# Performance work log

Measured on AMD Instinct MI355X. Metric: run time of the kernel, lower is better.

The kernel has to match this reference:

```python
import jax, jax.numpy as jnp
import numpy as np

B, L, D, H = 8, 1024, 768, 12
UNITS, NHEADS, HDIM = 768, 12, 64
R = 0.5  # ours_force_reduction_ratio
NEG = jnp.finfo(jnp.float32).min


def setup_inputs() -> dict:
    key = jax.random.key(0)
    ks = jax.random.split(key, 12)
    hidden_states = jax.random.normal(ks[0], (B, L, D), jnp.float32)
    # HF-style extended attention mask [B,1,1,L]: 0 for valid, big negative for padding
    lengths = jax.random.randint(ks[1], (B,), L // 2, L + 1)
    pos = jnp.arange(L)
    attention_mask = jnp.where(pos[None, :] < lengths[:, None], 0.0, -1e9).astype(jnp.float32).reshape(B, 1, 1, L)
    self_attention_scores = jax.random.uniform(ks[2], (B, H, L, L), dtype=jnp.float32)
    key_layer = jax.random.normal(ks[3], (B, H, L, HDIM), jnp.float32)  # unused by forward
    tome_size = jnp.ones((B, L, 1), jnp.float32)  # unused by forward (recomputed)
    s = 0.02
    Wq = jax.random.normal(ks[4], (D, UNITS), jnp.float32) * s
    Wk = jax.random.normal(ks[5], (D, UNITS), jnp.float32) * s
    Wv = jax.random.normal(ks[6], (D, UNITS), jnp.float32) * s
    Wo = jax.random.normal(ks[7], (UNITS, D), jnp.float32) * s
    bq = jnp.zeros((UNITS,), jnp.float32)
    bk = jnp.zeros((UNITS,), jnp.float32)
    bv = jnp.zeros((UNITS,), jnp.float32)
    bo = jnp.zeros((D,), jnp.float32)
    return dict(hidden_states=hidden_states, attention_mask=attention_mask,
                self_attention_scores=self_attention_scores, key_layer=key_layer,
                tome_size=tome_size, Wq=Wq, bq=bq, Wk=Wk, bk=bk, Wv=Wv, bv=bv, Wo=Wo, bo=bo)


def _mha(q, kv, key_padding_mask, Wq, bq, Wk, bk, Wv, bv, Wo, bo):
    # standard multi-head cross attention; q: [B,Lq,D], kv: [B,L,D]
    Bq, Lq, _ = q.shape
    Q = (q @ Wq + bq).reshape(Bq, Lq, NHEADS, HDIM)
    Kp = (kv @ Wk + bk).reshape(Bq, -1, NHEADS, HDIM)
    Vp = (kv @ Wv + bv).reshape(Bq, -1, NHEADS, HDIM)
    scores = jnp.einsum('bqhd,bkhd->bhqk', Q, Kp) / jnp.sqrt(jnp.float32(HDIM))
    if key_padding_mask is not None:
        scores = jnp.where(key_padding_mask[:, None, None, :], NEG, scores)
    att = jax.nn.softmax(scores, axis=-1)
    out = jnp.einsum('bhqk,bkhd->bqhd', att, Vp).reshape(Bq, Lq, UNITS)
    return out @ Wo + bo


def reference(hidden_states, attention_mask, self_attention_scores, key_layer, tome_size,
              Wq, bq, Wk, bk, Wv, bv, Wo, bo):
    # per-sample variable K = floor(valid_len * R) - num_new_token, clamped to >= 1
    valid = (attention_mask > -10.0).astype(hidden_states.dtype)  # [B,1,1,L]
    K_list = (valid.reshape(B, L).sum(-1) * R).astype(jnp.int32)
    K_list = jnp.maximum(K_list - 1, 1)  # num_new_token == 1
    # masked_attention_scores: outer product of the 0/1 mask applied per head
    m = valid.reshape(B, L)
    scores = self_attention_scores * (m[:, :, None] * m[:, None, :])[:, None, :, :]
    imp = scores.mean(axis=1).mean(axis=1)  # mean over heads then queries -> [B,L]
    imp = imp.at[:, 0].set(jnp.inf)  # always preserve CLS
    # rank of each token in descending importance (double argsort)
    order = jnp.argsort(-imp, axis=-1)
    rank = jnp.argsort(order, axis=-1)
    keep = rank < K_list[:, None]  # [B,L]; topk_attention_mask == ~keep
    preserved_attention_mask = jnp.where(keep[:, None, None, :], attention_mask, NEG)
    # sentence pooling via softmax over the extended mask
    att = jax.nn.softmax(attention_mask, axis=-1).reshape(B, 1, L)
    sentences = jnp.einsum('bql,bld->bqd', att, hidden_states)  # [B,1,D]
    key_padding_mask = attention_mask.reshape(B, L) < -10.0
    new_token = _mha(sentences, hidden_states, key_padding_mask, Wq, bq, Wk, bk, Wv, bv, Wo, bo)
    final_token = jnp.concatenate([hidden_states, new_token], axis=1)  # [B,L+1,D]
    new_attention_mask = jnp.zeros((B, 1, 1, 1), hidden_states.dtype)
    final_attention_mask = jnp.concatenate([preserved_attention_mask, new_attention_mask], axis=-1)
    tome = jnp.ones((B, L + 1, 1), hidden_states.dtype)
    return final_token, final_attention_mask, tome
```

## Files before the change

### kernel.cpp

```cpp
#include <hip/hip_runtime.h>
#include <math.h>

#define Bb 8
#define Ll 1024
#define Dd 768
#define Hh 12
#define ROWS7 32
#define QS 8
#define SS 8
#define WSC 16
#define DC 24

#define NIMP (Bb*Hh*QS)
#define NSENT (Bb*SS)
#define NCOPY4 (Bb*Ll*Dd/4)
#define NTOME4 (Bb*(Ll+1)/4)
#define NCPYBLK ((NCOPY4 + NTOME4 + 255)/256)
#define GRID_A (NIMP + NSENT + NCPYBLK + 1)

__device__ __constant__ float NEGF_ = -3.0e38f;

#define OFF_COUNTS   0
#define OFF_QPART    256
#define OFF_QV       (OFF_QPART + DC*Bb*Dd*4)
#define OFF_U        (OFF_QV + Bb*Dd*4)
#define OFF_SBUF     (OFF_U + Bb*Hh*Dd*4)
#define OFF_SENTP    (OFF_SBUF + (size_t)Bb*Hh*Ll*4)
#define OFF_PART     (OFF_SENTP + Bb*SS*Dd*8)
#define OFF_WPART    (OFF_PART + (size_t)Bb*Hh*QS*Ll*4)
#define OFF_OPART    (OFF_WPART + (size_t)Bb*WSC*Hh*Dd*4)
#define OFF_NPART    (OFF_OPART + DC*Bb*Dd*4)

__device__ __forceinline__ int block_count256(const float* __restrict__ amask_b, int t) {
    int c = 0;
    #pragma unroll
    for (int i = 0; i < 4; ++i)
        c += (amask_b[t + 256*i] > -10.0f) ? 1 : 0;
    #pragma unroll
    for (int off = 32; off; off >>= 1) c += __shfl_xor(c, off, 64);
    __shared__ int cred[4];
    if ((t & 63) == 0) cred[t >> 6] = c;
    __syncthreads();
    return cred[0] + cred[1] + cred[2] + cred[3];
}

__global__ void kA_mega(const float4* __restrict__ scores4, const float* __restrict__ amask,
                        const float4* __restrict__ hid4,
                        float4* __restrict__ part4, double* __restrict__ sentp,
                        int* __restrict__ counts, float4* __restrict__ out4) {
    int blk = blockIdx.x;
    int t = threadIdx.x;
    if (blk < NIMP) {
        int b = blk / (Hh*QS);
        int rem = blk % (Hh*QS);
        int h = rem / QS, c = rem % QS;
        int count = block_count256(amask + b*Ll, t);
        int rpc = (count + QS - 1) / QS;
        int q0 = c*rpc, q1 = min(q0 + rpc, count);
        const float4* base = scores4 + ((size_t)(b*Hh + h)*Ll)*(Ll/4) + t;
        float ax=0.f, ay=0.f, az=0.f, aw=0.f;
        float bx=0.f, by=0.f, bz=0.f, bw=0.f;
        int q = q0;
        #pragma unroll 4
        for (; q + 1 < q1; q += 2) {
            float4 v0 = base[(size_t)q*(Ll/4)];
            float4 v1 = base[(size_t)(q+1)*(Ll/4)];
            ax += v0.x; ay += v0.y; az += v0.z; aw += v0.w;
            bx += v1.x; by += v1.y; bz += v1.z; bw += v1.w;
        }
        if (q < q1) {
            float4 v = base[(size_t)q*(Ll/4)];
            ax += v.x; ay += v.y; az += v.z; aw += v.w;
        }
        float4 o; o.x = ax+bx; o.y = ay+by; o.z = az+bz; o.w = aw+bw;
        part4[(size_t)(b*(Hh*QS) + rem)*(Ll/4) + t] = o;
    } else if (blk < NIMP + NSENT) {
        int blk2 = blk - NIMP;
        int b = blk2 / SS, c = blk2 % SS;
        int count = block_count256(amask + b*Ll, t);
        int rpc = (count + SS - 1) / SS;
        int l0 = c*rpc, l1 = min(l0 + rpc, count);
        if (t < 192) {
            double a0=0, a1=0, a2=0, a3=0;
            const float4* base = hid4 + (size_t)b*Ll*(Dd/4) + t;
            #pragma unroll 4
            for (int l = l0; l < l1; ++l) {
                float4 v = base[(size_t)l*(Dd/4)];
                a0 += (double)v.x; a1 += (double)v.y; a2 += (double)v.z; a3 += (double)v.w;
            }
            double* o = sentp + (size_t)(b*SS + c)*Dd + 4*t;
            o[0]=a0; o[1]=a1; o[2]=a2; o[3]=a3;
        }
    } else if (blk < NIMP + NSENT + NCPYBLK) {
        int idx = (blk - NIMP - NSENT)*256 + t;
        if (idx < NCOPY4) {
            int b = idx / (Ll*Dd/4), r = idx % (Ll*Dd/4);
            out4[(size_t)b*((Ll+1)*Dd/4) + r] = hid4[idx];
        } else if (idx < NCOPY4 + NTOME4) {
            float4 one; one.x=one.y=one.z=one.w = 1.0f;
            out4[(size_t)(Bb*(Ll+1)*Dd + Bb*(Ll+1))/4 + (idx - NCOPY4)] = one;
        }
    } else {
        int w = t >> 6, lane = t & 63;
        for (int b = w; b < Bb; b += 4) {
            int c = 0;
            #pragma unroll
            for (int i = 0; i < 16; ++i)
                c += (amask[b*Ll + lane + 64*i] > -10.0f) ? 1 : 0;
            #pragma unroll
            for (int off = 32; off; off >>= 1) c += __shfl_xor(c, off, 64);
            if (lane == 0) counts[b] = c;
        }
    }
}

__global__ void kB_rank(const float* __restrict__ part, const int* __restrict__ counts,
                        const float* __restrict__ amask, float* __restrict__ out_mask) {
    __shared__ double simp[Ll];
    int blk = blockIdx.x;
    int b = blk >> 4, seg = blk & 15;
    int t = threadIdx.x;
    int count = counts[b];
    #pragma unroll
    for (int i = 0; i < 4; ++i) {
        int k = t + 256*i;
        double v;
        if (k == 0) v = 1.0e300;
        else if (k < count) {
            double s = 0.0;
            #pragma unroll 4
            for (int j = 0; j < Hh*QS; ++j)
                s += (double)part[(size_t)(b*(Hh*QS) + j)*Ll + k];
            v = s * (1.0/12288.0);
        } else v = 0.0;
        simp[k] = v;
    }
    __syncthreads();
    int K = max((count >> 1) - 1, 1);
    int ti = seg*64 + (t >> 2);
    int prt = t & 3;
    double mv = simp[ti];
    int cnt = 0;
    int l0 = prt*256;
    #pragma unroll 4
    for (int j = 0; j < 256; ++j) {
        int l = l0 + j;
        double v = simp[l];
        cnt += (v > mv || (v == mv && l < ti)) ? 1 : 0;
    }
    cnt += __shfl_xor(cnt, 1, 64);
    cnt += __shfl_xor(cnt, 2, 64);
    if (prt == 0)
        out_mask[b*(Ll+1) + ti] = (cnt < K) ? amask[b*Ll + ti] : NEGF_;
    if (seg == 0 && t == 0) out_mask[b*(Ll+1) + Ll] = 0.0f;
}

__global__ void kC_qpart(const double* __restrict__ sentp, const int* __restrict__ counts,
                         const float* __restrict__ Wq, float* __restrict__ qpart) {
    __shared__ float s_lds[Bb][32];
    int blk = blockIdx.x, t = threadIdx.x;
    int d0 = blk*32;
    {
        int b = t >> 5, dd = t & 31;
        double s = 0.0;
        #pragma unroll
        for (int c = 0; c < SS; ++c)
            s += sentp[(size_t)(b*SS + c)*Dd + d0 + dd];
        s_lds[b][dd] = (float)(s / (double)counts[b]);
    }
    __syncthreads();
    float acc[Bb][3];
    #pragma unroll
    for (int b = 0; b < Bb; ++b) { acc[b][0]=0.f; acc[b][1]=0.f; acc[b][2]=0.f; }
    #pragma unroll 4
    for (int dd = 0; dd < 32; ++dd) {
        const float* wr = Wq + (size_t)(d0 + dd)*Dd;
        float w0 = wr[t], w1 = wr[t+256], w2 = wr[t+512];
        #pragma unroll
        for (int b = 0; b < Bb; ++b) {
            float sv = s_lds[b][dd];
            acc[b][0] += sv*w0; acc[b][1] += sv*w1; acc[b][2] += sv*w2;
        }
    }
    #pragma unroll
    for (int b = 0; b < Bb; ++b) {
        float* o = qpart + (size_t)(blk*Bb + b)*Dd;
        o[t] = acc[b][0]; o[t+256] = acc[b][1]; o[t+512] = acc[b][2];
    }
}

__global__ void kD_u(const float* __restrict__ qpart, const float* __restrict__ bq,
                     const float* __restrict__ Wk,
                     float* __restrict__ Qv, float* __restrict__ u) {
    __shared__ float q_lds[64];
    int blk = blockIdx.x; int b = blk / Hh, h = blk % Hh;
    int t = threadIdx.x;
    if (t < 64) {
        int j = h*64 + t;
        float s = 0.f;
        #pragma unroll
        for (int c = 0; c < DC; ++c) s += qpart[(size_t)(c*Bb + b)*Dd + j];
        s += bq[j];
        q_lds[t] = s;
        Qv[b*Dd + j] = s;
    }
    __syncthreads();
    #pragma unroll
    for (int i = 0; i < 3; ++i) {
        int d = t + 256*i;
        const float* wr = Wk + (size_t)d*Dd + h*64;
        float acc = 0.f;
        #pragma unroll
        for (int j = 0; j < 64; ++j) acc += wr[j]*q_lds[j];
        u[(size_t)(b*Hh + h)*Dd + d] = acc;
    }
}

__global__ void kE_scores(const float4* __restrict__ hid4, const float4* __restrict__ u4,
                          const float* __restrict__ Qv, const float* __restrict__ bk,
                          const int* __restrict__ counts, float* __restrict__ sbuf) {
    __shared__ float4 u_lds[Hh*192];
    __shared__ float qbk[Hh];
    int blk = blockIdx.x;
    int b = blk / (Ll/ROWS7);
    int kc = blk % (Ll/ROWS7);
    int t = threadIdx.x;
    for (int i = t; i < Hh*192; i += 256) u_lds[i] = u4[(size_t)b*Hh*192 + i];
    if (t < Hh) {
        float a = 0.f;
        for (int j = 0; j < 64; ++j) a += Qv[b*Dd + t*64 + j] * bk[t*64 + j];
        qbk[t] = a;
    }
    __syncthreads();
    int count = counts[b];
    int wave = t >> 6, lane = t & 63;
    #pragma unroll
    for (int r = 0; r < ROWS7/4; ++r) {
        int k = kc*ROWS7 + wave + 4*r;
        const float4* hr4 = hid4 + (size_t)(b*Ll + k)*(Dd/4) + lane;
        float a[Hh];
        #pragma unroll
        for (int h = 0; h < Hh; ++h) a[h] = 0.f;
        #pragma unroll
        for (int i = 0; i < 3; ++i) {
            float4 v = hr4[i*64];
            #pragma unroll
            for (int h = 0; h < Hh; ++h) {
                float4 uv = u_lds[h*192 + i*64 + lane];
                a[h] += v.x*uv.x + v.y*uv.y + v.z*uv.z + v.w*uv.w;
            }
        }
        #pragma unroll
        for (int h = 0; h < Hh; ++h) {
            #pragma unroll
            for (int off = 32; off; off >>= 1) a[h] += __shfl_xor(a[h], off, 64);
        }
        #pragma unroll
        for (int h = 0; h < Hh; ++h) {
            if (lane == h) {
                sbuf[(size_t)(b*Hh + h)*Ll + k] =
                    (k < count) ? (a[h] + qbk[h]) * 0.125f : -1.0e30f;
            }
        }
    }
}

__global__ void kF_softmax(float* __restrict__ sbuf) {
    __shared__ float redmax[4];
    __shared__ float redsum[4];
    int blk = blockIdx.x, t = threadIdx.x;
    float* s = sbuf + (size_t)blk * Ll;
    int wave = t >> 6, lane = t & 63;
    float v0 = s[t], v1 = s[t+256], v2 = s[t+512], v3 = s[t+768];
    float mx = fmaxf(fmaxf(v0, v1), fmaxf(v2, v3));
    #pragma unroll
    for (int off = 32; off; off >>= 1) mx = fmaxf(mx, __shfl_xor(mx, off, 64));
    if (lane == 0) redmax[wave] = mx;
    __syncthreads();
    mx = fmaxf(fmaxf(redmax[0], redmax[1]), fmaxf(redmax[2], redmax[3]));
    float e0 = expf(v0-mx), e1 = expf(v1-mx), e2 = expf(v2-mx), e3 = expf(v3-mx);
    float sum = e0+e1+e2+e3;
    #pragma unroll
    for (int off = 32; off; off >>= 1) sum += __shfl_xor(sum, off, 64);
    if (lane == 0) redsum[wave] = sum;
    __syncthreads();
    sum = redsum[0]+redsum[1]+redsum[2]+redsum[3];
    s[t]     = e0/sum;
    s[t+256] = e1/sum;
    s[t+512] = e2/sum;
    s[t+768] = e3/sum;
}

__global__ void kG_wpart(const float4* __restrict__ hid4, const float* __restrict__ att,
                         const int* __restrict__ counts, float4* __restrict__ wpart4) {
    __shared__ float att_s[Hh][64];
    int blk = blockIdx.x;
    int b = blk / WSC, c = blk % WSC;
    int count = counts[b];
    int rpc = (count + WSC - 1) / WSC;
    int l0 = c*rpc, l1 = min(l0 + rpc, count);
    int nl = l1 - l0;
    int t = threadIdx.x;
    for (int idx = t; idx < Hh*64; idx += 192) {
        int h = idx >> 6, ll = idx & 63;
        att_s[h][ll] = (ll < nl) ? att[(size_t)(b*Hh + h)*Ll + l0 + ll] : 0.f;
    }
    __syncthreads();
    float4 acc[Hh];
    #pragma unroll
    for (int h = 0; h < Hh; ++h) { acc[h].x=0.f; acc[h].y=0.f; acc[h].z=0.f; acc[h].w=0.f; }
    const float4* base = hid4 + (size_t)b*Ll*(Dd/4) + t;
    #pragma unroll 2
    for (int l = 0; l < nl; ++l) {
        float4 v = base[(size_t)(l0 + l)*(Dd/4)];
        #pragma unroll
        for (int h = 0; h < Hh; ++h) {
            float ah = att_s[h][l];
            acc[h].x += ah*v.x; acc[h].y += ah*v.y; acc[h].z += ah*v.z; acc[h].w += ah*v.w;
        }
    }
    #pragma unroll
    for (int h = 0; h < Hh; ++h)
        wpart4[((size_t)(b*WSC + c)*Hh + h)*(Dd/4) + t] = acc[h];
}

__global__ void kH_opart(const float* __restrict__ wpart, const float* __restrict__ Wv,
                         float* __restrict__ opart) {
    __shared__ float w_lds[Bb][Hh][32];
    int blk = blockIdx.x, t = threadIdx.x;
    int d0 = blk*32;
    for (int idx = t; idx < Bb*Hh*32; idx += 256) {
        int b = idx / (Hh*32);
        int rem = idx % (Hh*32);
        int h = rem >> 5, dd = rem & 31;
        float s = 0.f;
        #pragma unroll
        for (int c = 0; c < WSC; ++c)
            s += wpart[((size_t)(b*WSC + c)*Hh + h)*Dd + d0 + dd];
        w_lds[b][h][dd] = s;
    }
    __syncthreads();
    int j0 = t, j1 = t+256, j2 = t+512;
    int h0 = j0 >> 6, h1 = j1 >> 6, h2 = j2 >> 6;
    float acc[Bb][3];
    #pragma unroll
    for (int b = 0; b < Bb; ++b) { acc[b][0]=0.f; acc[b][1]=0.f; acc[b][2]=0.f; }
    #pragma unroll 4
    for (int dd = 0; dd < 32; ++dd) {
        const float* wr = Wv + (size_t)(d0 + dd)*Dd;
        float w0 = wr[j0], w1 = wr[j1], w2 = wr[j2];
        #pragma unroll
        for (int b = 0; b < Bb; ++b) {
            acc[b][0] += w_lds[b][h0][dd]*w0;
            acc[b][1] += w_lds[b][h1][dd]*w1;
            acc[b][2] += w_lds[b][h2][dd]*w2;
        }
    }
    #pragma unroll
    for (int b = 0; b < Bb; ++b) {
        float* o = opart + (size_t)(blk*Bb + b)*Dd;
        o[j0] = acc[b][0]; o[j1] = acc[b][1]; o[j2] = acc[b][2];
    }
}

__global__ void kI_npart(const float* __restrict__ opart, const float* __restrict__ bv,
                         const float* __restrict__ Wo, float* __restrict__ npart) {
    __shared__ float o_lds[Bb][32];
    int blk = blockIdx.x, t = threadIdx.x;
    int jr0 = blk*32;
    {
        int b = t >> 5, jj = t & 31;
        int j = jr0 + jj;
        float s = 0.f;
        #pragma unroll
        for (int c = 0; c < DC; ++c) s += opart[(size_t)(c*Bb + b)*Dd + j];
        o_lds[b][jj] = s + bv[j];
    }
    __syncthreads();
    float acc[Bb][3];
    #pragma unroll
    for (int b = 0; b < Bb; ++b) { acc[b][0]=0.f; acc[b][1]=0.f; acc[b][2]=0.f; }
    #pragma unroll 4
    for (int jj = 0; jj < 32; ++jj) {
        const float* wr = Wo + (size_t)(jr0 + jj)*Dd;
        float w0 = wr[t], w1 = wr[t+256], w2 = wr[t+512];
        #pragma unroll
        for (int b = 0; b < Bb; ++b) {
            float ov = o_lds[b][jj];
            acc[b][0] += ov*w0; acc[b][1] += ov*w1; acc[b][2] += ov*w2;
        }
    }
    #pragma unroll
    for (int b = 0; b < Bb; ++b) {
        float* o = npart + (size_t)(blk*Bb + b)*Dd;
        o[t] = acc[b][0]; o[t+256] = acc[b][1]; o[t+512] = acc[b][2];
    }
}

__global__ void kJ_final(const float* __restrict__ npart, const float* __restrict__ bo,
                         float* __restrict__ out) {
    int b = blockIdx.x, t = threadIdx.x;
    size_t base = ((size_t)b*(Ll+1) + Ll)*Dd;
    #pragma unroll
    for (int i = 0; i < 3; ++i) {
        int d = t + 256*i;
        float s = 0.f;
        #pragma unroll
        for (int c = 0; c < DC; ++c) s += npart[(size_t)(c*Bb + b)*Dd + d];
        out[base + d] = s + bo[d];
    }
}

extern "C" void kernel_launch(void* const* d_in, const int* in_sizes, int n_in,
                              void* d_out, int out_size, void* d_ws, size_t ws_size,
                              hipStream_t stream) {
    const float* hidden = (const float*)d_in[0];
    const float* amask  = (const float*)d_in[1];
    const float* scores = (const float*)d_in[2];
    const float* Wq = (const float*)d_in[5];
    const float* bq = (const float*)d_in[6];
    const float* Wk = (const float*)d_in[7];
    const float* bk = (const float*)d_in[8];
    const float* Wv = (const float*)d_in[9];
    const float* bv = (const float*)d_in[10];
    const float* Wo = (const float*)d_in[11];
    const float* bo = (const float*)d_in[12];
    float* out = (float*)d_out;

    char* ws = (char*)d_ws;
    int*    counts = (int*)   (ws + OFF_COUNTS);
    float*  qpart  = (float*) (ws + OFF_QPART);
    float*  Qv     = (float*) (ws + OFF_QV);
    float*  u      = (float*) (ws + OFF_U);
    float*  sbuf   = (float*) (ws + OFF_SBUF);
    double* sentp  = (double*)(ws + OFF_SENTP);
    float*  part   = (float*) (ws + OFF_PART);
    float*  wpart  = (float*) (ws + OFF_WPART);
    float*  opart  = (float*) (ws + OFF_OPART);
    float*  npart  = (float*) (ws + OFF_NPART);

    float* out_mask = out + (size_t)Bb*(Ll+1)*Dd;

    kA_mega   <<<GRID_A, 256, 0, stream>>>((const float4*)scores, amask,
                                           (const float4*)hidden,
                                           (float4*)part, sentp, counts, (float4*)out);
    kB_rank   <<<Bb*16, 256, 0, stream>>>(part, counts, amask, out_mask);
    kC_qpart  <<<DC, 256, 0, stream>>>(sentp, counts, Wq, qpart);
    kD_u      <<<Bb*Hh, 256, 0, stream>>>(qpart, bq, Wk, Qv, u);
    kE_scores <<<Bb*(Ll/ROWS7), 256, 0, stream>>>((const float4*)hidden, (const float4*)u,
                                                  Qv, bk, counts, sbuf);
    kF_softmax<<<Bb*Hh, 256, 0, stream>>>(sbuf);
    kG_wpart  <<<Bb*WSC, 192, 0, stream>>>((const float4*)hidden, sbuf, counts,
                                           (float4*)wpart);
    kH_opart  <<<DC, 256, 0, stream>>>(wpart, Wv, opart);
    kI_npart  <<<DC, 256, 0, stream>>>(opart, bv, Wo, npart);
    kJ_final  <<<Bb, 256, 0, stream>>>(npart, bo, out);
}
```

Baseline: 209.6 us.

## Fuse small attention stages, fold softmax into wpart, skip padded score columns

```diff
diff --git a/kernel.cpp b/kernel.cpp
--- a/kernel.cpp
+++ b/kernel.cpp
@@ -21,15 +21,13 @@
 __device__ __constant__ float NEGF_ = -3.0e38f;
 
 #define OFF_COUNTS   0
-#define OFF_QPART    256
-#define OFF_QV       (OFF_QPART + DC*Bb*Dd*4)
-#define OFF_U        (OFF_QV + Bb*Dd*4)
-#define OFF_SBUF     (OFF_U + Bb*Hh*Dd*4)
-#define OFF_SENTP    (OFF_SBUF + (size_t)Bb*Hh*Ll*4)
-#define OFF_PART     (OFF_SENTP + Bb*SS*Dd*8)
-#define OFF_WPART    (OFF_PART + (size_t)Bb*Hh*QS*Ll*4)
-#define OFF_OPART    (OFF_WPART + (size_t)Bb*WSC*Hh*Dd*4)
-#define OFF_NPART    (OFF_OPART + DC*Bb*Dd*4)
+#define OFF_QBK      256
+#define OFF_OBUF     1024
+#define OFF_U        25600
+#define OFF_SENTP    320512
+#define OFF_SBUF     713728
+#define OFF_PART     1106944
+#define OFF_WPART    4252672
 
 __device__ __forceinline__ int block_count256(const float* __restrict__ amask_b, int t) {
     int c = 0;
@@ -57,6 +55,7 @@
         int count = block_count256(amask + b*Ll, t);
         int rpc = (count + QS - 1) / QS;
         int q0 = c*rpc, q1 = min(q0 + rpc, count);
+        if (4*t >= count) return;
         const float4* base = scores4 + ((size_t)(b*Hh + h)*Ll)*(Ll/4) + t;
         float ax=0.f, ay=0.f, az=0.f, aw=0.f;
         float bx=0.f, by=0.f, bz=0.f, bw=0.f;
@@ -114,123 +113,110 @@
     }
 }
 
-__global__ void kB_rank(const float* __restrict__ part, const int* __restrict__ counts,
-                        const float* __restrict__ amask, float* __restrict__ out_mask) {
+__global__ void kBCD(const float* __restrict__ part, const double* __restrict__ sentp,
+                     const int* __restrict__ counts, const float* __restrict__ amask,
+                     const float* __restrict__ Wq, const float* __restrict__ bq,
+                     const float* __restrict__ Wk, const float* __restrict__ bk,
+                     float* __restrict__ out_mask, float* __restrict__ u,
+                     float* __restrict__ qbk) {
     __shared__ double simp[Ll];
+    __shared__ float s_lds[Dd];
+    __shared__ float qpart_lds[4][64];
+    __shared__ float q_lds[64];
     int blk = blockIdx.x;
-    int b = blk >> 4, seg = blk & 15;
     int t = threadIdx.x;
-    int count = counts[b];
-    #pragma unroll
-    for (int i = 0; i < 4; ++i) {
-        int k = t + 256*i;
-        double v;
-        if (k == 0) v = 1.0e300;
-        else if (k < count) {
+    if (blk < 128) {
+        int b = blk >> 4, seg = blk & 15;
+        int count = counts[b];
+        #pragma unroll
+        for (int i = 0; i < 4; ++i) {
+            int k = t + 256*i;
+            double v;
+            if (k == 0) v = 1.0e300;
+            else if (k < count) {
+                double s = 0.0;
+                #pragma unroll 4
+                for (int j = 0; j < Hh*QS; ++j)
+                    s += (double)part[(size_t)(b*(Hh*QS) + j)*Ll + k];
+                v = s * (1.0/12288.0);
+            } else v = 0.0;
+            simp[k] = v;
+        }
+        __syncthreads();
+        int K = max((count >> 1) - 1, 1);
+        int ti = seg*64 + (t >> 2);
+        int prt = t & 3;
+        double mv = simp[ti];
+        int cnt = 0;
+        int l0 = prt*256;
+        #pragma unroll 4
+        for (int j = 0; j < 256; ++j) {
+            int l = l0 + j;
+            double v = simp[l];
+            cnt += (v > mv || (v == mv && l < ti)) ? 1 : 0;
+        }
+        cnt += __shfl_xor(cnt, 1, 64);
+        cnt += __shfl_xor(cnt, 2, 64);
+        if (prt == 0)
+            out_mask[b*(Ll+1) + ti] = (cnt < K) ? amask[b*Ll + ti] : NEGF_;
+        if (seg == 0 && t == 0) out_mask[b*(Ll+1) + Ll] = 0.0f;
+    } else {
+        int idx = blk - 128;
+        int b = idx / Hh, h = idx % Hh;
+        double cntd = (double)counts[b];
+        for (int i = t; i < Dd; i += 256) {
             double s = 0.0;
+            #pragma unroll
+            for (int c = 0; c < SS; ++c) s += sentp[(size_t)(b*SS + c)*Dd + i];
+            s_lds[i] = (float)(s / cntd);
+        }
+        __syncthreads();
+        {
+            int j = t & 63, g = t >> 6;
+            float acc = 0.f;
+            const float* wq = Wq + h*64 + j;
+            int d0 = g*192;
             #pragma unroll 4
-            for (int j = 0; j < Hh*QS; ++j)
-                s += (double)part[(size_t)(b*(Hh*QS) + j)*Ll + k];
-            v = s * (1.0/12288.0);
-        } else v = 0.0;
-        simp[k] = v;
-    }
-    __syncthreads();
-    int K = max((count >> 1) - 1, 1);
-    int ti = seg*64 + (t >> 2);
-    int prt = t & 3;
-    double mv = simp[ti];
-    int cnt = 0;
-    int l0 = prt*256;
-    #pragma unroll 4
-    for (int j = 0; j < 256; ++j) {
-        int l = l0 + j;
-        double v = simp[l];
-        cnt += (v > mv || (v == mv && l < ti)) ? 1 : 0;
-    }
-    cnt += __shfl_xor(cnt, 1, 64);
-    cnt += __shfl_xor(cnt, 2, 64);
-    if (prt == 0)
-        out_mask[b*(Ll+1) + ti] = (cnt < K) ? amask[b*Ll + ti] : NEGF_;
-    if (seg == 0 && t == 0) out_mask[b*(Ll+1) + Ll] = 0.0f;
-}
-
-__global__ void kC_qpart(const double* __restrict__ sentp, const int* __restrict__ counts,
-                         const float* __restrict__ Wq, float* __restrict__ qpart) {
-    __shared__ float s_lds[Bb][32];
-    int blk = blockIdx.x, t = threadIdx.x;
-    int d0 = blk*32;
-    {
-        int b = t >> 5, dd = t & 31;
-        double s = 0.0;
-        #pragma unroll
-        for (int c = 0; c < SS; ++c)
-            s += sentp[(size_t)(b*SS + c)*Dd + d0 + dd];
-        s_lds[b][dd] = (float)(s / (double)counts[b]);
-    }
-    __syncthreads();
-    float acc[Bb][3];
-    #pragma unroll
-    for (int b = 0; b < Bb; ++b) { acc[b][0]=0.f; acc[b][1]=0.f; acc[b][2]=0.f; }
-    #pragma unroll 4
-    for (int dd = 0; dd < 32; ++dd) {
-        const float* wr = Wq + (size_t)(d0 + dd)*Dd;
-        float w0 = wr[t], w1 = wr[t+256], w2 = wr[t+512];
-        #pragma unroll
-        for (int b = 0; b < Bb; ++b) {
-            float sv = s_lds[b][dd];
-            acc[b][0] += sv*w0; acc[b][1] += sv*w1; acc[b][2] += sv*w2;
-        }
-    }
-    #pragma unroll
-    for (int b = 0; b < Bb; ++b) {
-        float* o = qpart + (size_t)(blk*Bb + b)*Dd;
-        o[t] = acc[b][0]; o[t+256] = acc[b][1]; o[t+512] = acc[b][2];
-    }
-}
-
-__global__ void kD_u(const float* __restrict__ qpart, const float* __restrict__ bq,
-                     const float* __restrict__ Wk,
-                     float* __restrict__ Qv, float* __restrict__ u) {
-    __shared__ float q_lds[64];
-    int blk = blockIdx.x; int b = blk / Hh, h = blk % Hh;
-    int t = threadIdx.x;
-    if (t < 64) {
-        int j = h*64 + t;
-        float s = 0.f;
-        #pragma unroll
-        for (int c = 0; c < DC; ++c) s += qpart[(size_t)(c*Bb + b)*Dd + j];
-        s += bq[j];
-        q_lds[t] = s;
-        Qv[b*Dd + j] = s;
-    }
-    __syncthreads();
-    #pragma unroll
-    for (int i = 0; i < 3; ++i) {
-        int d = t + 256*i;
-        const float* wr = Wk + (size_t)d*Dd + h*64;
-        float acc = 0.f;
-        #pragma unroll
-        for (int j = 0; j < 64; ++j) acc += wr[j]*q_lds[j];
-        u[(size_t)(b*Hh + h)*Dd + d] = acc;
+            for (int d = d0; d < d0 + 192; ++d)
+                acc += s_lds[d] * wq[(size_t)d*Dd];
+            qpart_lds[g][j] = acc;
+        }
+        __syncthreads();
+        if (t < 64) {
+            float q = qpart_lds[0][t] + qpart_lds[1][t] + qpart_lds[2][t]
+                    + qpart_lds[3][t] + bq[h*64 + t];
+            q_lds[t] = q;
+        }
+        __syncthreads();
+        if (t == 0) {
+            float a = 0.f;
+            #pragma unroll
+            for (int jj = 0; jj < 64; ++jj) a += q_lds[jj]*bk[h*64 + jj];
+            qbk[b*Hh + h] = a;
+        }
+        #pragma unroll
+        for (int i = 0; i < 3; ++i) {
+            int d = t + 256*i;
+            const float* wr = Wk + (size_t)d*Dd + h*64;
+            float acc = 0.f;
+            #pragma unroll
+            for (int jj = 0; jj < 64; ++jj) acc += wr[jj]*q_lds[jj];
+            u[(size_t)(b*Hh + h)*Dd + d] = acc;
+        }
     }
 }
 
 __global__ void kE_scores(const float4* __restrict__ hid4, const float4* __restrict__ u4,
-                          const float* __restrict__ Qv, const float* __restrict__ bk,
-                          const int* __restrict__ counts, float* __restrict__ sbuf) {
+                          const float* __restrict__ qbk, const int* __restrict__ counts,
+                          float* __restrict__ sbuf) {
     __shared__ float4 u_lds[Hh*192];
-    __shared__ float qbk[Hh];
+    __shared__ float qbk_lds[Hh];
     int blk = blockIdx.x;
     int b = blk / (Ll/ROWS7);
     int kc = blk % (Ll/ROWS7);
     int t = threadIdx.x;
     for (int i = t; i < Hh*192; i += 256) u_lds[i] = u4[(size_t)b*Hh*192 + i];
-    if (t < Hh) {
-        float a = 0.f;
-        for (int j = 0; j < 64; ++j) a += Qv[b*Dd + t*64 + j] * bk[t*64 + j];
-        qbk[t] = a;
-    }
+    if (t < Hh) qbk_lds[t] = qbk[b*Hh + t];
     __syncthreads();
     int count = counts[b];
     int wave = t >> 6, lane = t & 63;
@@ -259,51 +245,46 @@
         for (int h = 0; h < Hh; ++h) {
             if (lane == h) {
                 sbuf[(size_t)(b*Hh + h)*Ll + k] =
-                    (k < count) ? (a[h] + qbk[h]) * 0.125f : -1.0e30f;
+                    (k < count) ? (a[h] + qbk_lds[h]) * 0.125f : -1.0e30f;
             }
         }
     }
 }
 
-__global__ void kF_softmax(float* __restrict__ sbuf) {
-    __shared__ float redmax[4];
-    __shared__ float redsum[4];
-    int blk = blockIdx.x, t = threadIdx.x;
-    float* s = sbuf + (size_t)blk * Ll;
-    int wave = t >> 6, lane = t & 63;
-    float v0 = s[t], v1 = s[t+256], v2 = s[t+512], v3 = s[t+768];
-    float mx = fmaxf(fmaxf(v0, v1), fmaxf(v2, v3));
-    #pragma unroll
-    for (int off = 32; off; off >>= 1) mx = fmaxf(mx, __shfl_xor(mx, off, 64));
-    if (lane == 0) redmax[wave] = mx;
-    __syncthreads();
-    mx = fmaxf(fmaxf(redmax[0], redmax[1]), fmaxf(redmax[2], redmax[3]));
-    float e0 = expf(v0-mx), e1 = expf(v1-mx), e2 = expf(v2-mx), e3 = expf(v3-mx);
-    float sum = e0+e1+e2+e3;
-    #pragma unroll
-    for (int off = 32; off; off >>= 1) sum += __shfl_xor(sum, off, 64);
-    if (lane == 0) redsum[wave] = sum;
-    __syncthreads();
-    sum = redsum[0]+redsum[1]+redsum[2]+redsum[3];
-    s[t]     = e0/sum;
-    s[t+256] = e1/sum;
-    s[t+512] = e2/sum;
-    s[t+768] = e3/sum;
-}
-
-__global__ void kG_wpart(const float4* __restrict__ hid4, const float* __restrict__ att,
-                         const int* __restrict__ counts, float4* __restrict__ wpart4) {
+__global__ void kGp_wpart(const float4* __restrict__ hid4, const float* __restrict__ sbuf,
+                          const int* __restrict__ counts, float4* __restrict__ wpart4) {
+    __shared__ float m_s[Hh], is_s[Hh];
     __shared__ float att_s[Hh][64];
     int blk = blockIdx.x;
     int b = blk / WSC, c = blk % WSC;
+    int t = threadIdx.x;
+    int wave = t >> 6, lane = t & 63;
+    #pragma unroll
+    for (int i = 0; i < 4; ++i) {
+        int h = wave*4 + i;
+        const float* s = sbuf + (size_t)(b*Hh + h)*Ll;
+        float vals[16];
+        float mx = -INFINITY;
+        #pragma unroll
+        for (int q = 0; q < 16; ++q) { vals[q] = s[lane + 64*q]; mx = fmaxf(mx, vals[q]); }
+        #pragma unroll
+        for (int off = 32; off; off >>= 1) mx = fmaxf(mx, __shfl_xor(mx, off, 64));
+        float sum = 0.f;
+        #pragma unroll
+        for (int q = 0; q < 16; ++q) sum += expf(vals[q] - mx);
+        #pragma unroll
+        for (int off = 32; off; off >>= 1) sum += __shfl_xor(sum, off, 64);
+        if (lane == 0) { m_s[h] = mx; is_s[h] = 1.f/sum; }
+    }
+    __syncthreads();
     int count = counts[b];
     int rpc = (count + WSC - 1) / WSC;
     int l0 = c*rpc, l1 = min(l0 + rpc, count);
     int nl = l1 - l0;
-    int t = threadIdx.x;
     for (int idx = t; idx < Hh*64; idx += 192) {
         int h = idx >> 6, ll = idx & 63;
-        att_s[h][ll] = (ll < nl) ? att[(size_t)(b*Hh + h)*Ll + l0 + ll] : 0.f;
+        att_s[h][ll] = (ll < nl)
+            ? expf(sbuf[(size_t)(b*Hh + h)*Ll + l0 + ll] - m_s[h]) * is_s[h] : 0.f;
     }
     __syncthreads();
     float4 acc[Hh];
@@ -324,91 +305,66 @@
         wpart4[((size_t)(b*WSC + c)*Hh + h)*(Dd/4) + t] = acc[h];
 }
 
-__global__ void kH_opart(const float* __restrict__ wpart, const float* __restrict__ Wv,
-                         float* __restrict__ opart) {
-    __shared__ float w_lds[Bb][Hh][32];
+__global__ void kHp_out(const float* __restrict__ wpart, const float* __restrict__ Wv,
+                        const float* __restrict__ bv, float* __restrict__ obuf) {
+    __shared__ float w_lds[Bb][Dd];
+    __shared__ float red[8][32][Bb];
+    int blk = blockIdx.x, t = threadIdx.x;
+    int h = blk >> 1, j0 = blk*32;
+    for (int idx = t; idx < Bb*Dd; idx += 256) {
+        int b = idx / Dd, d = idx % Dd;
+        float s = 0.f;
+        #pragma unroll
+        for (int c = 0; c < WSC; ++c)
+            s += wpart[((size_t)(b*WSC + c)*Hh + h)*Dd + d];
+        w_lds[b][d] = s;
+    }
+    __syncthreads();
+    int jj = t & 31, g = t >> 5;
+    float acc[Bb];
+    #pragma unroll
+    for (int b = 0; b < Bb; ++b) acc[b] = 0.f;
+    for (int d = g; d < Dd; d += 8) {
+        float wv = Wv[(size_t)d*Dd + j0 + jj];
+        #pragma unroll
+        for (int b = 0; b < Bb; ++b) acc[b] += w_lds[b][d]*wv;
+    }
+    #pragma unroll
+    for (int b = 0; b < Bb; ++b) red[g][jj][b] = acc[b];
+    __syncthreads();
+    int b2 = t >> 5, jj2 = t & 31;
+    float s = 0.f;
+    #pragma unroll
+    for (int g2 = 0; g2 < 8; ++g2) s += red[g2][jj2][b2];
+    obuf[b2*Dd + j0 + jj2] = s + bv[j0 + jj2];
+}
+
+__global__ void kIp_final(const float* __restrict__ obuf, const float* __restrict__ Wo,
+                          const float* __restrict__ bo, float* __restrict__ out) {
+    __shared__ float o_lds[Bb][Dd];
+    __shared__ float red[8][32][Bb];
     int blk = blockIdx.x, t = threadIdx.x;
     int d0 = blk*32;
-    for (int idx = t; idx < Bb*Hh*32; idx += 256) {
-        int b = idx / (Hh*32);
-        int rem = idx % (Hh*32);
-        int h = rem >> 5, dd = rem & 31;
-        float s = 0.f;
-        #pragma unroll
-        for (int c = 0; c < WSC; ++c)
-            s += wpart[((size_t)(b*WSC + c)*Hh + h)*Dd + d0 + dd];
-        w_lds[b][h][dd] = s;
-    }
-    __syncthreads();
-    int j0 = t, j1 = t+256, j2 = t+512;
-    int h0 = j0 >> 6, h1 = j1 >> 6, h2 = j2 >> 6;
-    float acc[Bb][3];
-    #pragma unroll
-    for (int b = 0; b < Bb; ++b) { acc[b][0]=0.f; acc[b][1]=0.f; acc[b][2]=0.f; }
-    #pragma unroll 4
-    for (int dd = 0; dd < 32; ++dd) {
-        const float* wr = Wv + (size_t)(d0 + dd)*Dd;
-        float w0 = wr[j0], w1 = wr[j1], w2 = wr[j2];
-        #pragma unroll
-        for (int b = 0; b < Bb; ++b) {
-            acc[b][0] += w_lds[b][h0][dd]*w0;
-            acc[b][1] += w_lds[b][h1][dd]*w1;
-            acc[b][2] += w_lds[b][h2][dd]*w2;
-        }
-    }
-    #pragma unroll
-    for (int b = 0; b < Bb; ++b) {
-        float* o = opart + (size_t)(blk*Bb + b)*Dd;
-        o[j0] = acc[b][0]; o[j1] = acc[b][1]; o[j2] = acc[b][2];
-    }
-}
-
-__global__ void kI_npart(const float* __restrict__ opart, const float* __restrict__ bv,
-                         const float* __restrict__ Wo, float* __restrict__ npart) {
-    __shared__ float o_lds[Bb][32];
-    int blk = blockIdx.x, t = threadIdx.x;
-    int jr0 = blk*32;
-    {
-        int b = t >> 5, jj = t & 31;
-        int j = jr0 + jj;
-        float s = 0.f;
-        #pragma unroll
-        for (int c = 0; c < DC; ++c) s += opart[(size_t)(c*Bb + b)*Dd + j];
-        o_lds[b][jj] = s + bv[j];
-    }
-    __syncthreads();
-    float acc[Bb][3];
-    #pragma unroll
-    for (int b = 0; b < Bb; ++b) { acc[b][0]=0.f; acc[b][1]=0.f; acc[b][2]=0.f; }
-    #pragma unroll 4
-    for (int jj = 0; jj < 32; ++jj) {
-        const float* wr = Wo + (size_t)(jr0 + jj)*Dd;
-        float w0 = wr[t], w1 = wr[t+256], w2 = wr[t+512];
-        #pragma unroll
-        for (int b = 0; b < Bb; ++b) {
-            float ov = o_lds[b][jj];
-            acc[b][0] += ov*w0; acc[b][1] += ov*w1; acc[b][2] += ov*w2;
-        }
-    }
-    #pragma unroll
-    for (int b = 0; b < Bb; ++b) {
-        float* o = npart + (size_t)(blk*Bb + b)*Dd;
-        o[t] = acc[b][0]; o[t+256] = acc[b][1]; o[t+512] = acc[b][2];
-    }
-}
-
-__global__ void kJ_final(const float* __restrict__ npart, const float* __restrict__ bo,
-                         float* __restrict__ out) {
-    int b = blockIdx.x, t = threadIdx.x;
-    size_t base = ((size_t)b*(Ll+1) + Ll)*Dd;
-    #pragma unroll
-    for (int i = 0; i < 3; ++i) {
-        int d = t + 256*i;
-        float s = 0.f;
-        #pragma unroll
-        for (int c = 0; c < DC; ++c) s += npart[(size_t)(c*Bb + b)*Dd + d];
-        out[base + d] = s + bo[d];
-    }
+    for (int idx = t; idx < Bb*Dd; idx += 256)
+        o_lds[idx / Dd][idx % Dd] = obuf[idx];
+    __syncthreads();
+    int dd = t & 31, g = t >> 5;
+    float acc[Bb];
+    #pragma unroll
+    for (int b = 0; b < Bb; ++b) acc[b] = 0.f;
+    for (int j = g; j < Dd; j += 8) {
+        float wv = Wo[(size_t)j*Dd + d0 + dd];
+        #pragma unroll
+        for (int b = 0; b < Bb; ++b) acc[b] += o_lds[b][j]*wv;
+    }
+    #pragma unroll
+    for (int b = 0; b < Bb; ++b) red[g][dd][b] = acc[b];
+    __syncthreads();
+    int b2 = t >> 5, dd2 = t & 31;
+    float s = 0.f;
+    #pragma unroll
+    for (int g2 = 0; g2 < 8; ++g2) s += red[g2][dd2][b2];
+    out[((size_t)b2*(Ll+1) + Ll)*Dd + d0 + dd2] = s + bo[d0 + dd2];
 }
 
 extern "C" void kernel_launch(void* const* d_in, const int* in_sizes, int n_in,
@@ -429,30 +385,25 @@
 
     char* ws = (char*)d_ws;
     int*    counts = (int*)   (ws + OFF_COUNTS);
-    float*  qpart  = (float*) (ws + OFF_QPART);
-    float*  Qv     = (float*) (ws + OFF_QV);
+    float*  qbk    = (float*) (ws + OFF_QBK);
+    float*  obuf   = (float*) (ws + OFF_OBUF);
     float*  u      = (float*) (ws + OFF_U);
+    double* sentp  = (double*)(ws + OFF_SENTP);
     float*  sbuf   = (float*) (ws + OFF_SBUF);
-    double* sentp  = (double*)(ws + OFF_SENTP);
     float*  part   = (float*) (ws + OFF_PART);
     float*  wpart  = (float*) (ws + OFF_WPART);
-    float*  opart  = (float*) (ws + OFF_OPART);
-    float*  npart  = (float*) (ws + OFF_NPART);
 
     float* out_mask = out + (size_t)Bb*(Ll+1)*Dd;
 
     kA_mega   <<<GRID_A, 256, 0, stream>>>((const float4*)scores, amask,
                                            (const float4*)hidden,
                                            (float4*)part, sentp, counts, (float4*)out);
-    kB_rank   <<<Bb*16, 256, 0, stream>>>(part, counts, amask, out_mask);
-    kC_qpart  <<<DC, 256, 0, stream>>>(sentp, counts, Wq, qpart);
-    kD_u      <<<Bb*Hh, 256, 0, stream>>>(qpart, bq, Wk, Qv, u);
+    kBCD      <<<128 + Bb*Hh, 256, 0, stream>>>(part, sentp, counts, amask,
+                                                Wq, bq, Wk, bk, out_mask, u, qbk);
     kE_scores <<<Bb*(Ll/ROWS7), 256, 0, stream>>>((const float4*)hidden, (const float4*)u,
-                                                  Qv, bk, counts, sbuf);
-    kF_softmax<<<Bb*Hh, 256, 0, stream>>>(sbuf);
-    kG_wpart  <<<Bb*WSC, 192, 0, stream>>>((const float4*)hidden, sbuf, counts,
+                                                  qbk, counts, sbuf);
+    kGp_wpart <<<Bb*WSC, 192, 0, stream>>>((const float4*)hidden, sbuf, counts,
                                            (float4*)wpart);
-    kH_opart  <<<DC, 256, 0, stream>>>(wpart, Wv, opart);
-    kI_npart  <<<DC, 256, 0, stream>>>(opart, bv, Wo, npart);
-    kJ_final  <<<Bb, 256, 0, stream>>>(npart, bo, out);
-}
+    kHp_out   <<<DC, 256, 0, stream>>>(wpart, Wv, bv, obuf);
+    kIp_final <<<DC, 256, 0, stream>>>(obuf, Wo, bo, out);
+}
```

After: 262.8 us. +25.3%, slower.
